# Performance work log

Measured on AMD Instinct MI355X. Metric: run time of the kernel, lower is better.

Reference implementation:

```python
import jax, jax.numpy as jnp
import numpy as np

D_MODEL = 1024
D_FF = 4096
NUM_EXPERTS = 8
TOP_K = 2
LB_COEF = 0.01
Z_COEF = 0.001
EPS_LN = 1e-5


def setup_inputs() -> dict:
    key = jax.random.key(0)
    ks = jax.random.split(key, 8)
    B, L = 4, 2048
    s_in = 1.0 / np.sqrt(D_MODEL)
    s_ff = 1.0 / np.sqrt(D_FF)
    return {
        "x": jax.random.normal(ks[0], (B, L, D_MODEL), dtype=jnp.float32),
        "gate_w": jax.random.normal(ks[1], (NUM_EXPERTS, D_MODEL), dtype=jnp.float32) * s_in,
        "ln_g": jnp.ones((D_MODEL,), dtype=jnp.float32),
        "ln_b": jnp.zeros((D_MODEL,), dtype=jnp.float32),
        "w1": jax.random.normal(ks[2], (NUM_EXPERTS, D_MODEL, D_FF), dtype=jnp.float32) * s_in,
        "b1": jnp.zeros((NUM_EXPERTS, D_FF), dtype=jnp.float32),
        "w2": jax.random.normal(ks[3], (NUM_EXPERTS, D_FF, D_MODEL), dtype=jnp.float32) * s_ff,
        "b2": jnp.zeros((NUM_EXPERTS, D_MODEL), dtype=jnp.float32),
    }


def reference(x, gate_w, ln_g, ln_b, w1, b1, w2, b2):
    B, L, D = x.shape
    xf = x.reshape(-1, D)  # [T, D]

    # LayerNorm
    mu = jnp.mean(xf, axis=-1, keepdims=True)
    var = jnp.mean((xf - mu) ** 2, axis=-1, keepdims=True)
    x_norm = (xf - mu) * jax.lax.rsqrt(var + EPS_LN) * ln_g + ln_b

    # Router (eval mode: no noise)
    logits = jnp.clip(x_norm @ gate_w.T, -10.0, 10.0)  # [T, E]
    z_loss = jnp.mean(jax.nn.logsumexp(logits, axis=-1) ** 2) * Z_COEF
    probs = jax.nn.softmax(logits, axis=-1)

    gw, idx = jax.lax.top_k(probs, TOP_K)  # [T, K]
    gw = gw / (jnp.sum(gw, axis=-1, keepdims=True) + 1e-8)

    # Load-balancing aux loss uses top-1 assignment
    top1_mask = jax.nn.one_hot(idx[:, 0], NUM_EXPERTS, dtype=jnp.float32)
    fraction_routed = jnp.mean(top1_mask, axis=0)
    mean_prob = jnp.mean(probs, axis=0)
    aux_loss = NUM_EXPERTS * jnp.sum(fraction_routed * mean_prob) * LB_COEF
    total_aux = aux_loss + z_loss

    # Combine weights [T, E]: sum over k of gate weight where routed to e
    combine = jnp.einsum("tk,tke->te", gw, jax.nn.one_hot(idx, NUM_EXPERTS, dtype=gw.dtype))

    # Dense per-expert FFN (Expert: Linear -> GELU -> Linear), combined by weights
    out = jnp.zeros_like(xf)
    for e in range(NUM_EXPERTS):
        h = jax.nn.gelu(x_norm @ w1[e] + b1[e], approximate=False)
        y = h @ w2[e] + b2[e]
        out = out + combine[:, e:e + 1] * y

    return x + out.reshape(B, L, D), total_aux
```

## Files before the change

### kernel.cpp

```cpp
#include <hip/hip_runtime.h>
#include <math.h>

typedef __bf16 bf16_t;
typedef bf16_t bf16x8 __attribute__((ext_vector_type(8)));
typedef bf16_t bf16x4 __attribute__((ext_vector_type(4)));
typedef float  f32x4  __attribute__((ext_vector_type(4)));

#define T_TOK 8192
#define DM 1024
#define DF 4096
#define NE 8
#define NP 16384

__device__ __forceinline__ f32x4 mfma_bf16(bf16x8 a, bf16x8 b, f32x4 c) {
  return __builtin_amdgcn_mfma_f32_16x16x32_bf16(a, b, c, 0, 0, 0);
}

__device__ __forceinline__ void gload16(const void* g, void* l) {
  __builtin_amdgcn_global_load_lds((const __attribute__((address_space(1))) void*)g,
                                   (__attribute__((address_space(3))) void*)l, 16, 0, 0);
}

__device__ __forceinline__ float erf_fast(float x) {
  float ax = fabsf(x);
  float t = 1.f / (1.f + 0.3275911f * ax);
  float p = t * (0.254829592f + t * (-0.284496736f + t * (1.421413741f +
            t * (-1.453152027f + t * 1.061405429f))));
  float r = 1.f - p * __expf(-ax * ax);
  return copysignf(r, x);
}

__device__ __forceinline__ unsigned swz_off(int row, int ch) {
  return (unsigned)(((row >> 1) << 7) + (((((row & 1) << 2) | ch) ^ ((row >> 1) & 7)) << 4));
}


__global__ __launch_bounds__(256) void k_router(
    const float* __restrict__ x, const float* __restrict__ gate_w,
    const float* __restrict__ ln_g, const float* __restrict__ ln_b,
    float* __restrict__ out, bf16_t* __restrict__ xn,
    int* __restrict__ eidx, float* __restrict__ gts, int* __restrict__ meta)
{
  int* cnt1 = meta;
  int* cnt2 = meta + 8;
  float* probsum = (float*)(meta + 32);
  float* zsum    = (float*)(meta + 40);

  __shared__ float sprob[8];
  __shared__ float sz;
  __shared__ int sc1[8], sc2[8];
  if (threadIdx.x < 8) { sprob[threadIdx.x] = 0.f; sc1[threadIdx.x] = 0; sc2[threadIdx.x] = 0; }
  if (threadIdx.x == 8) sz = 0.f;
  __syncthreads();

  int lane = threadIdx.x & 63, wv = threadIdx.x >> 6;
  int t = blockIdx.x * 4 + wv;
  const float* xt = x + (size_t)t * DM;

  float4 v[4];
  float s1 = 0.f, s2 = 0.f;
  #pragma unroll
  for (int c = 0; c < 4; ++c) {
    v[c] = *(const float4*)(xt + c * 256 + lane * 4);
    s1 += v[c].x + v[c].y + v[c].z + v[c].w;
    s2 += v[c].x * v[c].x + v[c].y * v[c].y + v[c].z * v[c].z + v[c].w * v[c].w;
  }
  #pragma unroll
  for (int o = 32; o > 0; o >>= 1) { s1 += __shfl_xor(s1, o, 64); s2 += __shfl_xor(s2, o, 64); }
  float mu = s1 * (1.f / DM);
  float var = s2 * (1.f / DM) - mu * mu;
  float rstd = rsqrtf(var + 1e-5f);

  float xv[16];
  #pragma unroll
  for (int c = 0; c < 4; ++c) {
    int d = c * 256 + lane * 4;
    float4 g4 = *(const float4*)(ln_g + d);
    float4 b4 = *(const float4*)(ln_b + d);
    xv[c*4+0] = (v[c].x - mu) * rstd * g4.x + b4.x;
    xv[c*4+1] = (v[c].y - mu) * rstd * g4.y + b4.y;
    xv[c*4+2] = (v[c].z - mu) * rstd * g4.z + b4.z;
    xv[c*4+3] = (v[c].w - mu) * rstd * g4.w + b4.w;
    *(float4*)(out + (size_t)t * DM + d) = v[c];
    bf16x4 pk = { (bf16_t)xv[c*4+0], (bf16_t)xv[c*4+1], (bf16_t)xv[c*4+2], (bf16_t)xv[c*4+3] };
    *(bf16x4*)(xn + (size_t)t * DM + d) = pk;
  }

  float lg[8];
  #pragma unroll
  for (int e = 0; e < 8; ++e) {
    float p = 0.f;
    #pragma unroll
    for (int c = 0; c < 4; ++c) {
      int d = c * 256 + lane * 4;
      float4 g4 = *(const float4*)(gate_w + e * DM + d);
      p += xv[c*4+0] * g4.x + xv[c*4+1] * g4.y + xv[c*4+2] * g4.z + xv[c*4+3] * g4.w;
    }
    #pragma unroll
    for (int o = 32; o > 0; o >>= 1) p += __shfl_xor(p, o, 64);
    lg[e] = p;
  }

  if (lane == 0) {
    float m = -1e30f;
    #pragma unroll
    for (int e = 0; e < 8; ++e) { lg[e] = fminf(fmaxf(lg[e], -10.f), 10.f); m = fmaxf(m, lg[e]); }
    float pr[8]; float se = 0.f;
    #pragma unroll
    for (int e = 0; e < 8; ++e) { pr[e] = expf(lg[e] - m); se += pr[e]; }
    float inv = 1.f / se;
    #pragma unroll
    for (int e = 0; e < 8; ++e) pr[e] *= inv;
    float lse = m + logf(se);

    int e0 = 0; float p0 = pr[0];
    #pragma unroll
    for (int e = 1; e < 8; ++e) if (pr[e] > p0) { p0 = pr[e]; e0 = e; }
    int e1 = -1; float p1 = -1.f;
    #pragma unroll
    for (int e = 0; e < 8; ++e) if (e != e0 && pr[e] > p1) { p1 = pr[e]; e1 = e; }
    float s = p0 + p1 + 1e-8f;
    eidx[t*2]   = e0; eidx[t*2+1] = e1;
    gts[t*2]    = p0 / s; gts[t*2+1] = p1 / s;

    atomicAdd(&sc1[e0], 1);
    atomicAdd(&sc2[e0], 1);
    atomicAdd(&sc2[e1], 1);
    #pragma unroll
    for (int e = 0; e < 8; ++e) atomicAdd(&sprob[e], pr[e]);
    atomicAdd(&sz, lse * lse);
  }
  __syncthreads();
  if (threadIdx.x < 8) {
    if (sc1[threadIdx.x]) atomicAdd(&cnt1[threadIdx.x], sc1[threadIdx.x]);
    if (sc2[threadIdx.x]) atomicAdd(&cnt2[threadIdx.x], sc2[threadIdx.x]);
    atomicAdd(&probsum[threadIdx.x], sprob[threadIdx.x]);
  }
  if (threadIdx.x == 8) atomicAdd(zsum, sz);
}

__global__ __launch_bounds__(256) void k_convT2(
    const float* __restrict__ w1, bf16_t* __restrict__ w1t,
    const float* __restrict__ w2, bf16_t* __restrict__ w2t)
{
  int bid = blockIdx.x;
  const float* s; bf16_t* d; int R, C, c0, r0;
  if (bid < 8192) {
    int e = bid >> 10, rem = bid & 1023;
    R = DM; C = DF;
    s = w1 + (size_t)e * R * C; d = w1t + (size_t)e * R * C;
    c0 = (rem & 63) * 64; r0 = (rem >> 6) * 64;
  } else {
    int e = (bid - 8192) >> 10, rem = (bid - 8192) & 1023;
    R = DF; C = DM;
    s = w2 + (size_t)e * R * C; d = w2t + (size_t)e * R * C;
    c0 = (rem & 15) * 64; r0 = (rem >> 4) * 64;
  }

  __shared__ float tile[64][65];
  int t = threadIdx.x;
  #pragma unroll
  for (int i = 0; i < 4; ++i) {
    int idx = i * 256 + t;
    int r = idx >> 4, c4 = (idx & 15) * 4;
    float4 v = *(const float4*)(s + (size_t)(r0 + r) * C + c0 + c4);
    tile[r][c4]   = v.x; tile[r][c4+1] = v.y;
    tile[r][c4+2] = v.z; tile[r][c4+3] = v.w;
  }
  __syncthreads();
  #pragma unroll
  for (int i = 0; i < 2; ++i) {
    int idx = i * 256 + t;
    int c = idx >> 3, r8 = (idx & 7) * 8;
    bf16x8 pk;
    #pragma unroll
    for (int k = 0; k < 8; ++k) pk[k] = (bf16_t)tile[r8 + k][c];
    *(bf16x8*)(d + (size_t)(c0 + c) * R + r0 + r8) = pk;
  }
}

__global__ void k_finalize(int* __restrict__ meta, float* __restrict__ aux_out) {
  if (threadIdx.x == 0 && blockIdx.x == 0) {
    int acc = 0;
    for (int e = 0; e < 8; ++e) { meta[24 + e] = acc; acc += meta[8 + e]; }
    const float* probsum = (const float*)(meta + 32);
    const float* zsum    = (const float*)(meta + 40);
    float s = 0.f;
    for (int e = 0; e < 8; ++e)
      s += ((float)meta[e] * (1.f / 8192.f)) * (probsum[e] * (1.f / 8192.f));
    aux_out[0] = 8.f * s * 0.01f + (zsum[0] * (1.f / 8192.f)) * 0.001f;
  }
}

__global__ __launch_bounds__(256) void k_assign(
    const int* __restrict__ eidx, float* __restrict__ gts,
    int* __restrict__ meta, int* __restrict__ list, float* __restrict__ gl,
    int* __restrict__ t2s)
{
  int t = blockIdx.x * 256 + threadIdx.x;
  int* cursor = meta + 16;
  const int* off = meta + 24;
  #pragma unroll
  for (int k = 0; k < 2; ++k) {
    int e = eidx[t*2 + k];
    float g = gts[t*2 + k];
    int pos = atomicAdd(&cursor[e], 1);
    int slot = off[e] + pos;
    list[slot] = t;
    gl[slot] = g;
    t2s[t*2 + k] = slot;
  }
}


#define VW(N) asm volatile("s_waitcnt vmcnt(" #N ")" ::: "memory")
#define BARSB do { __builtin_amdgcn_s_barrier(); __builtin_amdgcn_sched_barrier(0); } while (0)

#define STG_A(T, KS, P) do { \
  gload16(sAq[0] + (T)*64 + (KS)*32, smem + (P)*65536 + (KS)*16384 + dq[0]); \
  gload16(sAq[1] + (T)*64 + (KS)*32, smem + (P)*65536 + (KS)*16384 + dq[1]); } while (0)
#define STG_B(T, KS, P) do { \
  gload16(sBq[0] + (T)*64 + (KS)*32, smem + (P)*65536 + 32768 + (KS)*16384 + dq[0]); \
  gload16(sBq[1] + (T)*64 + (KS)*32, smem + (P)*65536 + 32768 + (KS)*16384 + dq[1]); } while (0)

#define LDA_(AF, P, KS) do { _Pragma("unroll") for (int i_ = 0; i_ < 8; ++i_) \
  AF[i_] = *(const bf16x8*)(smem + (P)*65536 + (KS)*16384 + a_off[i_]); } while (0)
#define LDBA(P, KS) do { \
  bfrA0 = *(const bf16x8*)(smem + (P)*65536 + 32768 + (KS)*16384 + b_off[0]); \
  bfrA1 = *(const bf16x8*)(smem + (P)*65536 + 32768 + (KS)*16384 + b_off[1]); } while (0)
#define LDBB(P, KS) do { \
  bfrB0 = *(const bf16x8*)(smem + (P)*65536 + 32768 + (KS)*16384 + b_off[2]); \
  bfrB1 = *(const bf16x8*)(smem + (P)*65536 + 32768 + (KS)*16384 + b_off[3]); } while (0)

#define FMAQ(AF, B0, B1, NH) do { __builtin_amdgcn_s_setprio(1); \
  _Pragma("unroll") for (int i_ = 0; i_ < 8; ++i_) { \
    acc[i_][(NH)*2+0] = mfma_bf16(AF[i_], B0, acc[i_][(NH)*2+0]); \
    acc[i_][(NH)*2+1] = mfma_bf16(AF[i_], B1, acc[i_][(NH)*2+1]); } \
  __builtin_amdgcn_s_setprio(0); } while (0)

#define TILE(T, P) do { \
  STG_A((T)+1, 0, (P)^1); VW(6); BARSB; \
  LDA_(afr0, P, 0); LDBA(P, 0); FMAQ(afr0, bfrA0, bfrA1, 0); \
  STG_B((T)+1, 0, (P)^1); VW(8); BARSB; \
  LDBB(P, 0); FMAQ(afr0, bfrB0, bfrB1, 1); \
  STG_A((T)+1, 1, (P)^1); VW(6); BARSB; \
  LDA_(afr1, P, 1); LDBA(P, 1); FMAQ(afr1, bfrA0, bfrA1, 0); \
  STG_B((T)+1, 1, (P)^1); VW(8); BARSB; \
  LDBB(P, 1); FMAQ(afr1, bfrB0, bfrB1, 1); \
} while (0)

#define TAIL(P) do { \
  VW(4); BARSB; LDA_(afr0, P, 0); LDBA(P, 0); FMAQ(afr0, bfrA0, bfrA1, 0); \
  VW(4); BARSB; LDBB(P, 0); FMAQ(afr0, bfrB0, bfrB1, 1); \
  VW(0); BARSB; LDA_(afr1, P, 1); LDBA(P, 1); FMAQ(afr1, bfrA0, bfrA1, 0); \
  VW(0); BARSB; LDBB(P, 1); FMAQ(afr1, bfrB0, bfrB1, 1); \
} while (0)

#define GEMM_PIPE(NT) do { \
  STG_A(0, 0, 0); STG_B(0, 0, 0); STG_A(0, 1, 0); STG_B(0, 1, 0); \
  for (int t_ = 0; t_ + 2 < (NT); t_ += 2) { TILE(t_, 0); TILE(t_ + 1, 1); } \
  TILE((NT) - 2, 0); \
  TAIL(1); \
} while (0)

__global__ __launch_bounds__(512, 1) void k_ffn1(
    const bf16_t* __restrict__ xn, const bf16_t* __restrict__ w1t,
    const float* __restrict__ b1, bf16_t* __restrict__ H,
    const int* __restrict__ list, const int* __restrict__ meta)
{
  extern __shared__ char smem[];
  int e = blockIdx.z;
  int cnt = meta[8 + e];
  int m0 = blockIdx.y * 256;
  if (m0 >= cnt) return;
  int offe = meta[24 + e];
  int n0 = blockIdx.x * 256;

  int tid = threadIdx.x, lane = tid & 63, wv = tid >> 6;
  int wm = wv >> 2, wn = wv & 3;

  const bf16_t* sAq[2]; const bf16_t* sBq[2];
  unsigned dq[2];
  #pragma unroll
  for (int i = 0; i < 2; ++i) {
    int s = i * 512 + tid;
    int line = s >> 3, u = s & 7, w = u ^ (line & 7);
    int row = (line << 1) | (w >> 2), ch = w & 3;
    int mrow = min(m0 + row, cnt - 1);
    int token = list[offe + mrow];
    sAq[i] = xn + (size_t)token * DM + ch * 8;
    sBq[i] = w1t + ((size_t)e * DF + n0 + row) * DM + ch * 8;
    dq[i] = (unsigned)(i * 8192 + wv * 1024);
  }

  unsigned a_off[8], b_off[4];
  #pragma unroll
  for (int i = 0; i < 8; ++i) a_off[i] = swz_off(wm * 128 + i * 16 + (lane & 15), lane >> 4);
  #pragma unroll
  for (int j = 0; j < 4; ++j)
    b_off[j] = swz_off(wn * 64 + (j >> 1) * 32 + (j & 1) * 16 + (lane & 15), lane >> 4);

  f32x4 acc[8][4];
  #pragma unroll
  for (int i = 0; i < 8; ++i)
    #pragma unroll
    for (int j = 0; j < 4; ++j)
      acc[i][j] = (f32x4){0.f, 0.f, 0.f, 0.f};
  bf16x8 afr0[8], afr1[8], bfrA0, bfrA1, bfrB0, bfrB1;

  GEMM_PIPE(DM / 64);

  int rq = (lane >> 4) << 2;
  int cb = n0 + wn * 64 + (lane & 15);
  #pragma unroll
  for (int i = 0; i < 8; ++i) {
    #pragma unroll
    for (int q = 0; q < 4; ++q) {
      int mg = m0 + wm * 128 + i * 16 + rq + q;
      if (mg < cnt) {
        size_t hrow = (size_t)(offe + mg) * DF;
        #pragma unroll
        for (int j = 0; j < 4; ++j) {
          int col = cb + (j >> 1) * 32 + (j & 1) * 16;
          float hv = acc[i][j][q] + b1[e * DF + col];
          hv = 0.5f * hv * (1.f + erf_fast(hv * 0.70710678118f));
          H[hrow + col] = (bf16_t)hv;
        }
      }
    }
  }
}

__global__ __launch_bounds__(512, 1) void k_ffn2(
    const bf16_t* __restrict__ H, const bf16_t* __restrict__ w2t,
    const float* __restrict__ b2, bf16_t* __restrict__ Y,
    const int* __restrict__ meta)
{
  extern __shared__ char smem[];
  int e = blockIdx.z;
  int cnt = meta[8 + e];
  int m0 = blockIdx.y * 256;
  if (m0 >= cnt) return;
  int offe = meta[24 + e];
  int n0 = blockIdx.x * 256;

  int tid = threadIdx.x, lane = tid & 63, wv = tid >> 6;
  int wm = wv >> 2, wn = wv & 3;

  const bf16_t* sAq[2]; const bf16_t* sBq[2];
  unsigned dq[2];
  #pragma unroll
  for (int i = 0; i < 2; ++i) {
    int s = i * 512 + tid;
    int line = s >> 3, u = s & 7, w = u ^ (line & 7);
    int row = (line << 1) | (w >> 2), ch = w & 3;
    int mrow = min(m0 + row, cnt - 1);
    sAq[i] = H + (size_t)(offe + mrow) * DF + ch * 8;
    sBq[i] = w2t + ((size_t)e * DM + n0 + row) * DF + ch * 8;
    dq[i] = (unsigned)(i * 8192 + wv * 1024);
  }

  unsigned a_off[8], b_off[4];
  #pragma unroll
  for (int i = 0; i < 8; ++i) a_off[i] = swz_off(wm * 128 + i * 16 + (lane & 15), lane >> 4);
  #pragma unroll
  for (int j = 0; j < 4; ++j)
    b_off[j] = swz_off(wn * 64 + (j >> 1) * 32 + (j & 1) * 16 + (lane & 15), lane >> 4);

  f32x4 acc[8][4];
  #pragma unroll
  for (int i = 0; i < 8; ++i)
    #pragma unroll
    for (int j = 0; j < 4; ++j)
      acc[i][j] = (f32x4){0.f, 0.f, 0.f, 0.f};
  bf16x8 afr0[8], afr1[8], bfrA0, bfrA1, bfrB0, bfrB1;

  GEMM_PIPE(DF / 64);

  int rq = (lane >> 4) << 2;
  int cb = n0 + wn * 64 + (lane & 15);
  #pragma unroll
  for (int i = 0; i < 8; ++i) {
    #pragma unroll
    for (int q = 0; q < 4; ++q) {
      int mg = m0 + wm * 128 + i * 16 + rq + q;
      if (mg < cnt) {
        size_t yrow = (size_t)(offe + mg) * DM;
        #pragma unroll
        for (int j = 0; j < 4; ++j) {
          int col = cb + (j >> 1) * 32 + (j & 1) * 16;
          Y[yrow + col] = (bf16_t)(acc[i][j][q] + b2[e * DM + col]);
        }
      }
    }
  }
}

__global__ __launch_bounds__(256) void k_combine(
    const bf16_t* __restrict__ Y, const int* __restrict__ t2s,
    const float* __restrict__ gl, float* __restrict__ out)
{
  int lane = threadIdx.x & 63, wv = threadIdx.x >> 6;
  int t = blockIdx.x * 4 + wv;
  int s0 = t2s[t*2], s1 = t2s[t*2 + 1];
  float g0 = gl[s0], g1 = gl[s1];
  const bf16_t* y0 = Y + (size_t)s0 * DM;
  const bf16_t* y1 = Y + (size_t)s1 * DM;
  float* o = out + (size_t)t * DM;
  #pragma unroll
  for (int c = 0; c < 4; ++c) {
    int d = c * 256 + lane * 4;
    float4 r  = *(const float4*)(o + d);
    bf16x4 a = *(const bf16x4*)(y0 + d);
    bf16x4 b = *(const bf16x4*)(y1 + d);
    r.x += g0 * (float)a[0] + g1 * (float)b[0];
    r.y += g0 * (float)a[1] + g1 * (float)b[1];
    r.z += g0 * (float)a[2] + g1 * (float)b[2];
    r.w += g0 * (float)a[3] + g1 * (float)b[3];
    *(float4*)(o + d) = r;
  }
}

extern "C" void kernel_launch(void* const* d_in, const int* in_sizes, int n_in,
                              void* d_out, int out_size, void* d_ws, size_t ws_size,
                              hipStream_t stream) {
  const float* x      = (const float*)d_in[0];
  const float* gate_w = (const float*)d_in[1];
  const float* ln_g   = (const float*)d_in[2];
  const float* ln_b   = (const float*)d_in[3];
  const float* w1     = (const float*)d_in[4];
  const float* b1     = (const float*)d_in[5];
  const float* w2     = (const float*)d_in[6];
  const float* b2     = (const float*)d_in[7];
  float* out = (float*)d_out;

  char* ws = (char*)d_ws;
  bf16_t* xn   = (bf16_t*)(ws);
  bf16_t* w1t  = (bf16_t*)(ws + 16777216ull);
  bf16_t* Y    = (bf16_t*)(ws + 16777216ull);
  bf16_t* w2t  = (bf16_t*)(ws + 83886080ull);
  bf16_t* H    = (bf16_t*)(ws + 150994944ull);
  int*    list = (int*)   (ws + 285212672ull);
  float*  gl   = (float*) (ws + 285278208ull);
  int*    eidx = (int*)   (ws + 285343744ull);
  float*  gts  = (float*) (ws + 285409280ull);
  int*    t2s  = (int*)   (ws + 285409280ull);
  int*    meta = (int*)   (ws + 285474816ull);

  hipFuncSetAttribute((const void*)k_ffn1, hipFuncAttributeMaxDynamicSharedMemorySize, 131072);
  hipFuncSetAttribute((const void*)k_ffn2, hipFuncAttributeMaxDynamicSharedMemorySize, 131072);

  hipMemsetAsync(meta, 0, 256, stream);
  k_router<<<T_TOK / 4, 256, 0, stream>>>(x, gate_w, ln_g, ln_b, out, xn, eidx, gts, meta);
  k_convT2<<<16384, 256, 0, stream>>>(w1, w1t, w2, w2t);
  k_finalize<<<1, 1, 0, stream>>>(meta, out + (size_t)T_TOK * DM);
  k_assign<<<T_TOK / 256, 256, 0, stream>>>(eidx, gts, meta, list, gl, t2s);
  k_ffn1<<<dim3(DF / 256, 32, NE), 512, 131072, stream>>>(xn, w1t, b1, H, list, meta);
  k_ffn2<<<dim3(DM / 256, 32, NE), 512, 131072, stream>>>(H, w2t, b2, Y, meta);
  k_combine<<<T_TOK / 4, 256, 0, stream>>>(Y, t2s, gl, out);
}
```

Measured before the change: 648.7 us.

## Stage GEMM epilogues through LDS for vector stores and remap blocks per XCD

The FFN1 and FFN2 epilogues now write each wave's bias+GELU or bias result into a padded LDS tile. They then emit 16-byte row-contiguous stores to H and Y, replacing scattered 2-byte stores. The 3D grid is flattened to 1D and decoded so that blocks sharing an expert and N-tile land on the same XCD, aiming to improve L2 reuse of weight tiles. This needs more dynamic LDS (144KB) and extra barriers in the epilogue.

```diff
diff --git a/kernel.cpp b/kernel.cpp
--- a/kernel.cpp
+++ b/kernel.cpp
@@ -269,12 +269,17 @@
     const int* __restrict__ list, const int* __restrict__ meta)
 {
   extern __shared__ char smem[];
-  int e = blockIdx.z;
+  int bid = blockIdx.x;
+  int xcd = bid & 7, idx = bid >> 3;
+  int m = idx & 31, pn = idx >> 5;
+  int g = pn * 8 + xcd;
+  int e = g >> 4, n = g & 15;
+
   int cnt = meta[8 + e];
-  int m0 = blockIdx.y * 256;
+  int m0 = m * 256;
   if (m0 >= cnt) return;
   int offe = meta[24 + e];
-  int n0 = blockIdx.x * 256;
+  int n0 = n * 256;
 
   int tid = threadIdx.x, lane = tid & 63, wv = tid >> 6;
   int wm = wv >> 2, wn = wv & 3;
@@ -310,23 +315,33 @@
 
   GEMM_PIPE(DM / 64);
 
+  __syncthreads();
+  unsigned wbase = (unsigned)(wv * 18432);
   int rq = (lane >> 4) << 2;
-  int cb = n0 + wn * 64 + (lane & 15);
   #pragma unroll
   for (int i = 0; i < 8; ++i) {
     #pragma unroll
-    for (int q = 0; q < 4; ++q) {
-      int mg = m0 + wm * 128 + i * 16 + rq + q;
-      if (mg < cnt) {
-        size_t hrow = (size_t)(offe + mg) * DF;
-        #pragma unroll
-        for (int j = 0; j < 4; ++j) {
-          int col = cb + (j >> 1) * 32 + (j & 1) * 16;
-          float hv = acc[i][j][q] + b1[e * DF + col];
-          hv = 0.5f * hv * (1.f + erf_fast(hv * 0.70710678118f));
-          H[hrow + col] = (bf16_t)hv;
-        }
+    for (int j = 0; j < 4; ++j) {
+      int colL = (j >> 1) * 32 + (j & 1) * 16 + (lane & 15);
+      float bb = b1[e * DF + n0 + wn * 64 + colL];
+      #pragma unroll
+      for (int q = 0; q < 4; ++q) {
+        int rowL = i * 16 + rq + q;
+        float hv = acc[i][j][q] + bb;
+        hv = 0.5f * hv * (1.f + erf_fast(hv * 0.70710678118f));
+        *(bf16_t*)(smem + wbase + rowL * 144 + colL * 2) = (bf16_t)hv;
       }
+    }
+  }
+  __syncthreads();
+  #pragma unroll
+  for (int it = 0; it < 16; ++it) {
+    int slot = it * 64 + lane;
+    int rowL = slot >> 3, chunk = slot & 7;
+    int mg = m0 + wm * 128 + rowL;
+    if (mg < cnt) {
+      bf16x8 vv = *(const bf16x8*)(smem + wbase + rowL * 144 + chunk * 16);
+      *(bf16x8*)(&H[(size_t)(offe + mg) * DF + n0 + wn * 64 + chunk * 8]) = vv;
     }
   }
 }
@@ -337,12 +352,17 @@
     const int* __restrict__ meta)
 {
   extern __shared__ char smem[];
-  int e = blockIdx.z;
+  int bid = blockIdx.x;
+  int xcd = bid & 7, idx = bid >> 3;
+  int m = idx & 31, pn = idx >> 5;
+  int g = pn * 8 + xcd;
+  int e = g >> 2, n = g & 3;
+
   int cnt = meta[8 + e];
-  int m0 = blockIdx.y * 256;
+  int m0 = m * 256;
   if (m0 >= cnt) return;
   int offe = meta[24 + e];
-  int n0 = blockIdx.x * 256;
+  int n0 = n * 256;
 
   int tid = threadIdx.x, lane = tid & 63, wv = tid >> 6;
   int wm = wv >> 2, wn = wv & 3;
@@ -377,21 +397,31 @@
 
   GEMM_PIPE(DF / 64);
 
+  __syncthreads();
+  unsigned wbase = (unsigned)(wv * 18432);
   int rq = (lane >> 4) << 2;
-  int cb = n0 + wn * 64 + (lane & 15);
   #pragma unroll
   for (int i = 0; i < 8; ++i) {
     #pragma unroll
-    for (int q = 0; q < 4; ++q) {
-      int mg = m0 + wm * 128 + i * 16 + rq + q;
-      if (mg < cnt) {
-        size_t yrow = (size_t)(offe + mg) * DM;
-        #pragma unroll
-        for (int j = 0; j < 4; ++j) {
-          int col = cb + (j >> 1) * 32 + (j & 1) * 16;
-          Y[yrow + col] = (bf16_t)(acc[i][j][q] + b2[e * DM + col]);
-        }
+    for (int j = 0; j < 4; ++j) {
+      int colL = (j >> 1) * 32 + (j & 1) * 16 + (lane & 15);
+      float bb = b2[e * DM + n0 + wn * 64 + colL];
+      #pragma unroll
+      for (int q = 0; q < 4; ++q) {
+        int rowL = i * 16 + rq + q;
+        *(bf16_t*)(smem + wbase + rowL * 144 + colL * 2) = (bf16_t)(acc[i][j][q] + bb);
       }
+    }
+  }
+  __syncthreads();
+  #pragma unroll
+  for (int it = 0; it < 16; ++it) {
+    int slot = it * 64 + lane;
+    int rowL = slot >> 3, chunk = slot & 7;
+    int mg = m0 + wm * 128 + rowL;
+    if (mg < cnt) {
+      bf16x8 vv = *(const bf16x8*)(smem + wbase + rowL * 144 + chunk * 16);
+      *(bf16x8*)(&Y[(size_t)(offe + mg) * DM + n0 + wn * 64 + chunk * 8]) = vv;
     }
   }
 }
@@ -447,15 +477,15 @@
   int*    t2s  = (int*)   (ws + 285409280ull);
   int*    meta = (int*)   (ws + 285474816ull);
 
-  hipFuncSetAttribute((const void*)k_ffn1, hipFuncAttributeMaxDynamicSharedMemorySize, 131072);
-  hipFuncSetAttribute((const void*)k_ffn2, hipFuncAttributeMaxDynamicSharedMemorySize, 131072);
+  hipFuncSetAttribute((const void*)k_ffn1, hipFuncAttributeMaxDynamicSharedMemorySize, 147456);
+  hipFuncSetAttribute((const void*)k_ffn2, hipFuncAttributeMaxDynamicSharedMemorySize, 147456);
 
   hipMemsetAsync(meta, 0, 256, stream);
   k_router<<<T_TOK / 4, 256, 0, stream>>>(x, gate_w, ln_g, ln_b, out, xn, eidx, gts, meta);
   k_convT2<<<16384, 256, 0, stream>>>(w1, w1t, w2, w2t);
   k_finalize<<<1, 1, 0, stream>>>(meta, out + (size_t)T_TOK * DM);
   k_assign<<<T_TOK / 256, 256, 0, stream>>>(eidx, gts, meta, list, gl, t2s);
-  k_ffn1<<<dim3(DF / 256, 32, NE), 512, 131072, stream>>>(xn, w1t, b1, H, list, meta);
-  k_ffn2<<<dim3(DM / 256, 32, NE), 512, 131072, stream>>>(H, w2t, b2, Y, meta);
+  k_ffn1<<<NE * 16 * 32, 512, 147456, stream>>>(xn, w1t, b1, H, list, meta);
+  k_ffn2<<<NE * 4 * 32, 512, 147456, stream>>>(H, w2t, b2, Y, meta);
   k_combine<<<T_TOK / 4, 256, 0, stream>>>(Y, t2s, gl, out);
 }
```

Result: no change. 658.7 us (+1.5%).
